# Performance work log

Hardware: AMD Instinct MI355X
Metric: run time of the kernel (lower is better)

The kernel has to match this reference:

```python
import jax, jax.numpy as jnp
import numpy as np

KD = 128; N_STU_TAB = 20000; N_EXER_TAB = 20000
NS = 4096; NE = 4096; NK = 128
E_SE = 131072; E_EK = 16384; B = 8192
ALPHAS = 0.1; ALPHAE = 0.1; TAU = 0.5


def setup_inputs():
    key = jax.random.key(0)
    ks = jax.random.split(key, 32)
    f = lambda i, shape, s=0.09: jax.random.normal(ks[i], shape, dtype=jnp.float32) * s
    ri = lambda i, shape, hi: jax.random.randint(ks[i], shape, 0, hi)
    inp = {
        'E_stu': f(0, (N_STU_TAB, KD), 0.1),
        'E_exer': f(1, (N_EXER_TAB, KD), 0.1),
        'E_k': f(2, (NK, KD), 0.1),
        'W1': f(3, (KD, KD)), 'a1s': f(4, (KD,)), 'a1d': f(5, (KD,)),
        'W2': f(6, (KD, KD)), 'a2s': f(7, (KD,)), 'a2d': f(8, (KD,)),
        'pW1': f(9, (KD, KD)), 'pW2': f(10, (KD, KD)),
        'pW3': f(11, (KD, KD)), 'pb3': jnp.zeros((KD,), jnp.float32),
        'kn_r': (jax.random.uniform(ks[12], (B, KD)) < 0.25).astype(jnp.float32) + 1e-3,
        'stu_ids': ri(13, (NS,), N_STU_TAB),
        'exer_ids': ri(14, (NE,), N_EXER_TAB),
        'k_ids': jnp.arange(NK),
    }
    j = 15
    for g in ('g0', 'g1', 'g2'):
        inp['se_src_' + g] = ri(j, (E_SE,), NS); j += 1
        inp['se_dst_' + g] = ri(j, (E_SE,), NE); j += 1
        inp['ek_src_' + g] = ri(j, (E_EK,), NE); j += 1
        inp['ek_dst_' + g] = ri(j, (E_EK,), NK); j += 1
    inp['stu_index'] = ri(j, (B,), NS); j += 1
    inp['exer_index'] = ri(j, (B,), NE)
    return inp


def _seg_softmax_agg(scores, msgs, dst, n):
    # numerically-stable softmax over edges grouped by destination node
    m = jax.ops.segment_max(scores, dst, num_segments=n)
    m = jnp.where(jnp.isfinite(m), m, 0.0)
    ex = jnp.exp(scores - m[dst])
    den = jax.ops.segment_sum(ex, dst, num_segments=n)
    alpha = ex / (den[dst] + 1e-16)
    return jax.ops.segment_sum(alpha[:, None] * msgs, dst, num_segments=n)


def _gat(emb, edges, W, a_s, a_d):
    # single-head GAT over hetero edges: stu<->exer, exer<->k
    hs, he, hk = emb['stu'] @ W, emb['exer'] @ W, emb['k'] @ W
    ss_s, ss_e, ss_k = hs @ a_s, he @ a_s, hk @ a_s   # src attention terms
    sd_s, sd_e, sd_k = hs @ a_d, he @ a_d, hk @ a_d   # dst attention terms
    se_src, se_dst, ek_src, ek_dst = edges
    lrelu = lambda x: jax.nn.leaky_relu(x, 0.2)
    # stu <- exer (reverse of stu->exer edges)
    sc = lrelu(ss_e[se_dst] + sd_s[se_src])
    new_s = jax.nn.elu(_seg_softmax_agg(sc, he[se_dst], se_src, NS))
    # exer <- stu  and  exer <- k (softmax spans both relations)
    sc1 = lrelu(ss_s[se_src] + sd_e[se_dst])
    sc2 = lrelu(ss_k[ek_dst] + sd_e[ek_src])
    sc = jnp.concatenate([sc1, sc2])
    msg = jnp.concatenate([hs[se_src], hk[ek_dst]])
    dst = jnp.concatenate([se_dst, ek_src])
    new_e = jax.nn.elu(_seg_softmax_agg(sc, msg, dst, NE))
    # k <- exer
    sc = lrelu(ss_e[ek_src] + sd_k[ek_dst])
    new_k = jax.nn.elu(_seg_softmax_agg(sc, he[ek_src], ek_dst, NK))
    return {'stu': new_s, 'exer': new_e, 'k': new_k}


def _closs(h1, h2):
    z1 = h1 / (jnp.linalg.norm(h1, axis=1, keepdims=True) + 1e-12)
    z2 = h2 / (jnp.linalg.norm(h2, axis=1, keepdims=True) + 1e-12)
    sim = z1 @ z2.T                      # [N, N] cosine similarity
    ex = jnp.exp(sim / TAU)
    pos = jnp.diagonal(ex)
    neg = ex.sum(axis=1) - pos           # off-diagonal sum
    return jnp.mean(-jnp.log(pos / (pos + neg)))


def reference(E_stu, E_exer, E_k, W1, a1s, a1d, W2, a2s, a2d,
              pW1, pW2, pW3, pb3, kn_r,
              stu_ids, exer_ids, k_ids,
              se_src_g0, se_dst_g0, ek_src_g0, ek_dst_g0,
              se_src_g1, se_dst_g1, ek_src_g1, ek_dst_g1,
              se_src_g2, se_dst_g2, ek_src_g2, ek_dst_g2,
              stu_index, exer_index):
    e0 = {'stu': E_stu[stu_ids], 'exer': E_exer[exer_ids], 'k': E_k[k_ids]}

    def run(edges):
        e1 = _gat(e0, edges, W1, a1s, a1d)
        return _gat(e1, edges, W2, a2s, a2d)

    main = run((se_src_g0, se_dst_g0, ek_src_g0, ek_dst_g0))
    v1 = run((se_src_g1, se_dst_g1, ek_src_g1, ek_dst_g1))
    v2 = run((se_src_g2, se_dst_g2, ek_src_g2, ek_dst_g2))

    closs = (ALPHAS * (_closs(v1['stu'], v2['stu']) + _closs(v2['stu'], v1['stu']))
             + ALPHAE * (_closs(v1['exer'], v2['exer']) + _closs(v2['exer'], v1['exer'])))

    bs = main['stu'][stu_index]          # [B, KD]
    be = main['exer'][exer_index]        # [B, KD]
    pref = jax.nn.sigmoid(bs @ pW1.T)
    diff = jax.nn.sigmoid(be @ pW2.T)
    o = jax.nn.sigmoid((pref - diff) @ pW3.T + pb3)
    out = (o * kn_r).sum(axis=1) / kn_r.sum(axis=1)
    return out[:, None], closs
```

## Files before the change

### kernel.cpp

```cpp
#include <hip/hip_runtime.h>
#include <hip/hip_bf16.h>
#include <math.h>

#define KD 128
#define NS 4096
#define NE 4096
#define NK 128
#define NNODE (NS + NE + NK)
#define ESE 131072
#define EEK 16384
#define NCSR (2*ESE + 2*EEK)
#define BQ 8192
#define RP (NNODE + 1)
#define HB 32

typedef __attribute__((ext_vector_type(8))) short short8;
typedef __attribute__((ext_vector_type(4))) float float4_;

__device__ __forceinline__ float lrelu_(float x){ return x >= 0.f ? x : 0.2f*x; }
__device__ __forceinline__ float elu_(float x){ return x > 0.f ? x : __expf(x) - 1.f; }
__device__ __forceinline__ float sigm_(float x){ return 1.f/(1.f + __expf(-x)); }
__device__ __forceinline__ float bf2f_(unsigned short u){
  union { unsigned int i; float f; } v; v.i = ((unsigned int)u) << 16; return v.f;
}
__device__ __forceinline__ unsigned short f2b_(float x){
  __hip_bfloat16 b = __float2bfloat16(x); return *(unsigned short*)&b;
}

struct EdgePtrs { const int* s_src[3]; const int* s_dst[3]; const int* e_src[3]; const int* e_dst[3]; };

__global__ __launch_bounds__(256)
void k_fuse1(EdgePtrs ep, int* __restrict__ part,
             const float* __restrict__ W1, const float* __restrict__ a1s,
             const float* __restrict__ a1d,
             unsigned short* __restrict__ hb0, float* __restrict__ ss0,
             float* __restrict__ sd0,
             const float* __restrict__ E_stu, const float* __restrict__ E_exer,
             const float* __restrict__ E_k, const int* __restrict__ sid,
             const int* __restrict__ eid, const int* __restrict__ kid,
             const float* __restrict__ pW1, const float* __restrict__ pW2,
             const float* __restrict__ pW3, float* __restrict__ pWT,
             const float* __restrict__ W2, unsigned short* __restrict__ w2b) {
  __shared__ __align__(16) char smem[NNODE*4];
  int bid = blockIdx.x, t = threadIdx.x;

  if (bid < 3*HB) {
    int* hcnt = (int*)smem;
    int g = bid / HB, b = bid % HB;
    for (int i = t; i < NNODE; i += 256) hcnt[i] = 0;
    __syncthreads();
    const int* ss_ = ep.s_src[g]; const int* sd_ = ep.s_dst[g];
    const int* es_ = ep.e_src[g]; const int* ed_ = ep.e_dst[g];
    int se0 = b*(ESE/HB);
    for (int i = se0 + t; i < se0 + ESE/HB; i += 256) {
      atomicAdd(&hcnt[ss_[i]], 1);
      atomicAdd(&hcnt[NS + sd_[i]], 1);
    }
    int ek0 = b*(EEK/HB);
    for (int i = ek0 + t; i < ek0 + EEK/HB; i += 256) {
      atomicAdd(&hcnt[NS + es_[i]], 1);
      atomicAdd(&hcnt[NS + NE + ed_[i]], 1);
    }
    __syncthreads();
    int* pp = part + ((size_t)g*HB + b)*NNODE;
    for (int i = t; i < NNODE; i += 256) pp[i] = hcnt[i];
    return;
  }

  if (bid < 3*HB + NNODE/32) {
    float (*ers)[KD] = (float(*)[KD])smem;
    int row0 = (bid - 3*HB)*32;
    int w = t >> 6, c = t & 63;
    for (int i = t; i < 32*KD; i += 256) {
      int r = i >> 7, k = i & 127;
      int gr = row0 + r;
      const float* srow;
      if (gr < NS)           srow = E_stu  + (size_t)sid[gr]*KD;
      else if (gr < NS + NE) srow = E_exer + (size_t)eid[gr - NS]*KD;
      else                   srow = E_k    + (size_t)kid[gr - NS - NE]*KD;
      ers[r][k] = srow[k];
    }
    __syncthreads();
    float acc0[8] = {0,0,0,0,0,0,0,0}, acc1[8] = {0,0,0,0,0,0,0,0};
    #pragma unroll 2
    for (int kc = 0; kc < KD; kc += 4) {
      float wa[4], wb[4];
      #pragma unroll
      for (int j = 0; j < 4; j++) {
        wa[j] = W1[(kc + j)*KD + c];
        wb[j] = W1[(kc + j)*KD + c + 64];
      }
      #pragma unroll
      for (int r = 0; r < 8; r++) {
        float4 e = *(const float4*)&ers[w*8 + r][kc];
        acc0[r] += e.x*wa[0] + e.y*wa[1] + e.z*wa[2] + e.w*wa[3];
        acc1[r] += e.x*wb[0] + e.y*wb[1] + e.z*wb[2] + e.w*wb[3];
      }
    }
    float as1 = a1s[c], as2 = a1s[c + 64], ad1 = a1d[c], ad2 = a1d[c + 64];
    #pragma unroll
    for (int r = 0; r < 8; r++) {
      int gr = row0 + w*8 + r;
      hb0[(size_t)gr*KD + c]      = f2b_(acc0[r]);
      hb0[(size_t)gr*KD + c + 64] = f2b_(acc1[r]);
      float s = acc0[r]*as1 + acc1[r]*as2;
      float d = acc0[r]*ad1 + acc1[r]*ad2;
      #pragma unroll
      for (int off = 32; off; off >>= 1) { s += __shfl_xor(s, off); d += __shfl_xor(d, off); }
      if (c == 0) { ss0[gr] = s; sd0[gr] = d; }
    }
    return;
  }

  {
    float (*tile)[33] = (float(*)[33])smem;
    int idx = bid - 3*HB - NNODE/32;
    int tx = t & 31, ty = t >> 5;
    if (idx < 48) {
      int m = idx >> 4, rem = idx & 15;
      int bx = (rem & 3)*32, by = (rem >> 2)*32;
      const float* src = m == 0 ? pW1 : (m == 1 ? pW2 : pW3);
      float* dst = pWT + m*KD*KD;
      for (int j = 0; j < 32; j += 8)
        tile[ty + j][tx] = src[(by + ty + j)*KD + bx + tx];
      __syncthreads();
      for (int j = 0; j < 32; j += 8)
        dst[(bx + ty + j)*KD + by + tx] = tile[tx][ty + j];
    } else {
      int rem = idx - 48;
      int bx = (rem & 3)*32, by = (rem >> 2)*32;
      for (int j = 0; j < 32; j += 8)
        tile[ty + j][tx] = W2[(by + ty + j)*KD + bx + tx];
      __syncthreads();
      for (int j = 0; j < 32; j += 8)
        w2b[(bx + ty + j)*KD + by + tx] = f2b_(tile[tx][ty + j]);
    }
  }
}

__global__ void k_sumpart(const int* __restrict__ part, int* __restrict__ cnt_all) {
  int idx = blockIdx.x*256 + threadIdx.x;
  if (idx >= 3*NNODE) return;
  int g = idx / NNODE, n = idx - g*NNODE;
  const int* pg = part + (size_t)g*HB*NNODE + n;
  int s = 0;
  #pragma unroll
  for (int b = 0; b < HB; b++) s += pg[(size_t)b*NNODE];
  cnt_all[idx] = s;
}

__global__ void k_scan(const int* __restrict__ cnt_all, int* __restrict__ rp_all) {
  __shared__ int sums[1024];
  const int CH = (NNODE + 1023) / 1024;
  int g = blockIdx.x, t = threadIdx.x;
  const int* cnt = cnt_all + g*NNODE;
  int* row_ptr = rp_all + g*RP;
  int base = t*CH;
  int local[CH];
  int s = 0;
  for (int j = 0; j < CH; j++) {
    int v = (base + j < NNODE) ? cnt[base + j] : 0;
    local[j] = s; s += v;
  }
  sums[t] = s; __syncthreads();
  for (int off = 1; off < 1024; off <<= 1) {
    int v = (t >= off) ? sums[t - off] : 0;
    __syncthreads();
    sums[t] += v;
    __syncthreads();
  }
  int excl = (t == 0) ? 0 : sums[t - 1];
  for (int j = 0; j < CH; j++)
    if (base + j < NNODE) row_ptr[base + j] = excl + local[j];
  if (t == 1023) row_ptr[NNODE] = sums[1023];
}

__global__ void k_boff(const int* __restrict__ part, const int* __restrict__ rp_all,
                       int* __restrict__ boff) {
  int idx = blockIdx.x*256 + threadIdx.x;
  if (idx >= 3*NNODE) return;
  int g = idx / NNODE, n = idx - g*NNODE;
  const int* pg = part + (size_t)g*HB*NNODE + n;
  int* bg = boff + (size_t)g*HB*NNODE + n;
  int acc = rp_all[g*RP + n];
  #pragma unroll
  for (int b = 0; b < HB; b++) {
    bg[(size_t)b*NNODE] = acc;
    acc += pg[(size_t)b*NNODE];
  }
}

__global__ __launch_bounds__(256)
void k_scatter(EdgePtrs ep, const int* __restrict__ boff, unsigned short* __restrict__ col_all) {
  __shared__ int cur[NNODE];
  int g = blockIdx.y, b = blockIdx.x, t = threadIdx.x;
  const int* bg = boff + ((size_t)g*HB + b)*NNODE;
  for (int i = t; i < NNODE; i += 256) cur[i] = bg[i];
  __syncthreads();
  const int* ss_ = ep.s_src[g]; const int* sd_ = ep.s_dst[g];
  const int* es_ = ep.e_src[g]; const int* ed_ = ep.e_dst[g];
  unsigned short* col = col_all + (size_t)g*NCSR;
  int se0 = b*(ESE/HB);
  for (int i = se0 + t; i < se0 + ESE/HB; i += 256) {
    int s = ss_[i], d = NS + sd_[i];
    col[atomicAdd(&cur[s], 1)] = (unsigned short)d;
    col[atomicAdd(&cur[d], 1)] = (unsigned short)s;
  }
  int ek0 = b*(EEK/HB);
  for (int i = ek0 + t; i < ek0 + EEK/HB; i += 256) {
    int s = NS + es_[i], d = NS + NE + ed_[i];
    col[atomicAdd(&cur[s], 1)] = (unsigned short)d;
    col[atomicAdd(&cur[d], 1)] = (unsigned short)s;
  }
}

__global__ __launch_bounds__(256)
void k_mgemm(const unsigned short* __restrict__ X, const unsigned short* __restrict__ WT,
             const float* __restrict__ a_s, const float* __restrict__ a_d,
             unsigned short* __restrict__ hb, float* __restrict__ ss,
             float* __restrict__ sd) {
  __shared__ unsigned short As[128*KD];
  __shared__ unsigned short Bs[128*KD];
  __shared__ float ssp[128][2], sdp[128][2];
  int t = threadIdx.x;
  const unsigned short* Arow = X + (size_t)blockIdx.x*128*KD;
  #pragma unroll
  for (int j = 0; j < 8; j++) {
    int G = t + j*256;
    int r = G >> 4, g = G & 15;
    int sw = g ^ (r & 15);
    *(float4*)&As[(r*16 + sw)*8] = *(const float4*)&Arow[(size_t)G*8];
    *(float4*)&Bs[(r*16 + sw)*8] = *(const float4*)&WT[(size_t)G*8];
  }
  __syncthreads();
  int w = t >> 6, lane = t & 63;
  int rw = (w >> 1)*64, cw = (w & 1)*64;
  int m15 = lane & 15, quad = lane >> 4;
  float4_ acc[4][4] = {};
  #pragma unroll
  for (int kq = 0; kq < 4; kq++) {
    short8 a[4], b[4];
    int g = kq*4 + quad;
    #pragma unroll
    for (int mi = 0; mi < 4; mi++) {
      int r = rw + mi*16 + m15;
      a[mi] = *(const short8*)&As[(r*16 + (g ^ (r & 15)))*8];
    }
    #pragma unroll
    for (int ni = 0; ni < 4; ni++) {
      int r = cw + ni*16 + m15;
      b[ni] = *(const short8*)&Bs[(r*16 + (g ^ (r & 15)))*8];
    }
    #pragma unroll
    for (int mi = 0; mi < 4; mi++)
      #pragma unroll
      for (int ni = 0; ni < 4; ni++)
        acc[mi][ni] = __builtin_amdgcn_mfma_f32_16x16x32_bf16(a[mi], b[ni], acc[mi][ni], 0, 0, 0);
  }
  int row0 = blockIdx.x*128;
  float asv[4], adv[4];
  #pragma unroll
  for (int ni = 0; ni < 4; ni++) {
    int gc = cw + ni*16 + m15;
    asv[ni] = a_s[gc]; adv[ni] = a_d[gc];
  }
  #pragma unroll
  for (int mi = 0; mi < 4; mi++) {
    #pragma unroll
    for (int reg = 0; reg < 4; reg++) {
      int lr = rw + mi*16 + quad*4 + reg;
      int gr = row0 + lr;
      float s = 0.f, d = 0.f;
      #pragma unroll
      for (int ni = 0; ni < 4; ni++) {
        float v = acc[mi][ni][reg];
        hb[(size_t)gr*KD + cw + ni*16 + m15] = f2b_(v);
        s += v*asv[ni]; d += v*adv[ni];
      }
      s += __shfl_xor(s, 1); d += __shfl_xor(d, 1);
      s += __shfl_xor(s, 2); d += __shfl_xor(d, 2);
      s += __shfl_xor(s, 4); d += __shfl_xor(d, 4);
      s += __shfl_xor(s, 8); d += __shfl_xor(d, 8);
      if (m15 == 0) { ssp[lr][w & 1] = s; sdp[lr][w & 1] = d; }
    }
  }
  __syncthreads();
  if (t < 128) {
    ss[row0 + t] = ssp[t][0] + ssp[t][1];
    sd[row0 + t] = sdp[t][0] + sdp[t][1];
  }
}

__global__ __launch_bounds__(256)
void k_head(const float* __restrict__ Wa, const float* __restrict__ Wb,
            const float* __restrict__ Wc,
            const float* __restrict__ pb, const float* __restrict__ knr,
            float* __restrict__ out, const float* __restrict__ pbuf,
            const float* __restrict__ g1,
            const int* __restrict__ i1, const int* __restrict__ i2) {
  constexpr int ROWS = 32, RPW = 8;
  __shared__ float ers[ROWS][KD];
  __shared__ float xs[ROWS][KD];
  int t = threadIdx.x;
  int row0 = blockIdx.x * ROWS;
  int w = t >> 6, c = t & 63;

  for (int i = t; i < ROWS*KD; i += 256) {
    int r = i >> 7, k = i & 127;
    ers[r][k] = g1[(size_t)i1[row0 + r]*KD + k];
  }
  __syncthreads();

  float acc0[RPW], acc1[RPW];
  #pragma unroll
  for (int r = 0; r < RPW; r++) { acc0[r] = 0.f; acc1[r] = 0.f; }
  #pragma unroll 2
  for (int kc = 0; kc < KD; kc += 4) {
    float wa[4], wb[4];
    #pragma unroll
    for (int j = 0; j < 4; j++) {
      wa[j] = Wa[(kc + j)*KD + c];
      wb[j] = Wa[(kc + j)*KD + c + 64];
    }
    #pragma unroll
    for (int r = 0; r < RPW; r++) {
      float4 e = *(const float4*)&ers[w*RPW + r][kc];
      acc0[r] += e.x*wa[0] + e.y*wa[1] + e.z*wa[2] + e.w*wa[3];
      acc1[r] += e.x*wb[0] + e.y*wb[1] + e.z*wb[2] + e.w*wb[3];
    }
  }
  #pragma unroll
  for (int r = 0; r < RPW; r++) {
    xs[w*RPW + r][c]      = sigm_(acc0[r]);
    xs[w*RPW + r][c + 64] = sigm_(acc1[r]);
  }
  __syncthreads();
  for (int i = t; i < ROWS*KD; i += 256) {
    int r = i >> 7, k = i & 127;
    ers[r][k] = g1[(size_t)(NS + i2[row0 + r])*KD + k];
  }
  __syncthreads();
  #pragma unroll
  for (int r = 0; r < RPW; r++) { acc0[r] = 0.f; acc1[r] = 0.f; }
  #pragma unroll 2
  for (int kc = 0; kc < KD; kc += 4) {
    float wa[4], wb[4];
    #pragma unroll
    for (int j = 0; j < 4; j++) {
      wa[j] = Wb[(kc + j)*KD + c];
      wb[j] = Wb[(kc + j)*KD + c + 64];
    }
    #pragma unroll
    for (int r = 0; r < RPW; r++) {
      float4 e = *(const float4*)&ers[w*RPW + r][kc];
      acc0[r] += e.x*wa[0] + e.y*wa[1] + e.z*wa[2] + e.w*wa[3];
      acc1[r] += e.x*wb[0] + e.y*wb[1] + e.z*wb[2] + e.w*wb[3];
    }
  }
  #pragma unroll
  for (int r = 0; r < RPW; r++) {
    xs[w*RPW + r][c]      -= sigm_(acc0[r]);
    xs[w*RPW + r][c + 64] -= sigm_(acc1[r]);
  }
  #pragma unroll
  for (int r = 0; r < RPW; r++) { acc0[r] = 0.f; acc1[r] = 0.f; }
  #pragma unroll 2
  for (int kc = 0; kc < KD; kc += 4) {
    float wa[4], wb[4];
    #pragma unroll
    for (int j = 0; j < 4; j++) {
      wa[j] = Wc[(kc + j)*KD + c];
      wb[j] = Wc[(kc + j)*KD + c + 64];
    }
    #pragma unroll
    for (int r = 0; r < RPW; r++) {
      float4 e = *(const float4*)&xs[w*RPW + r][kc];
      acc0[r] += e.x*wa[0] + e.y*wa[1] + e.z*wa[2] + e.w*wa[3];
      acc1[r] += e.x*wb[0] + e.y*wb[1] + e.z*wb[2] + e.w*wb[3];
    }
  }
  float b1 = pb[c], b2 = pb[c + 64];
  #pragma unroll
  for (int r = 0; r < RPW; r++) {
    int gr = row0 + w*RPW + r;
    float kr1 = knr[(size_t)gr*KD + c], kr2 = knr[(size_t)gr*KD + c + 64];
    float o1 = sigm_(acc0[r] + b1), o2 = sigm_(acc1[r] + b2);
    float num = o1*kr1 + o2*kr2, den = kr1 + kr2;
    #pragma unroll
    for (int off = 32; off; off >>= 1) { num += __shfl_xor(num, off); den += __shfl_xor(den, off); }
    if (c == 0) out[gr] = num/den;
  }
  if (blockIdx.x == 0 && w == 0) {
    int lane = t & 63;
    float v = (lane < 32) ? pbuf[lane] : 0.f;
    #pragma unroll
    for (int off = 32; off; off >>= 1) v += __shfl_xor(v, off);
    if (lane == 0) out[BQ] = 0.1f*v/(float)NS;
  }
}

__global__ __launch_bounds__(256)
void k_agg(const int* __restrict__ rp_all, const unsigned short* __restrict__ col_all,
           const unsigned short* __restrict__ hb_base, const float* __restrict__ ss,
           const float* __restrict__ sd, unsigned short* __restrict__ outb,
           float* __restrict__ out, unsigned short* __restrict__ Zo, int gsel) {
  int wv = blockIdx.x*4 + (threadIdx.x >> 6);
  int lane = threadIdx.x & 63;
  if (wv >= 3*NNODE) return;
  int g = wv / NNODE, node = wv - g*NNODE;
  bool layer2 = (gsel == -2);
  if (layer2 && node >= NS + NE) return;
  const int* rp = rp_all + g*RP;
  const unsigned short* cl = col_all + (size_t)g*NCSR;
  const unsigned short* hgb = layer2 ? hb_base + (size_t)g*NNODE*KD : hb_base;
  const float* ssg = layer2 ? ss + g*NNODE : ss;
  const float* sdg = layer2 ? sd + g*NNODE : sd;
  int e0 = rp[node], e1 = rp[node + 1];
  float sdv = sdg[node];
  int sub = lane >> 4;
  int fl  = lane & 15;
  float l = 0.f;
  float A[8] = {0,0,0,0,0,0,0,0};
  #pragma unroll 4
  for (int e = e0 + sub; e < e1; e += 4) {
    int o = cl[e];
    float pj = __expf(lrelu_(ssg[o] + sdv));
    l += pj;
    short8 mv = *(const short8*)&hgb[(size_t)o*KD + fl*8];
    #pragma unroll
    for (int q = 0; q < 8; q++)
      A[q] += pj * bf2f_((unsigned short)mv[q]);
  }
  l += __shfl_xor(l, 16); l += __shfl_xor(l, 32);
  #pragma unroll
  for (int q = 0; q < 8; q++) {
    A[q] += __shfl_xor(A[q], 16);
    A[q] += __shfl_xor(A[q], 32);
  }
  float inv = 1.f/(l + 1e-16f);
  float av[8];
  #pragma unroll
  for (int q = 0; q < 8; q++) av[q] = elu_(A[q]*inv);
  if (!layer2) {
    if (sub == 0) {
      short8 sv;
      #pragma unroll
      for (int q = 0; q < 8; q++) sv[q] = (short)f2b_(av[q]);
      *(short8*)&outb[(size_t)wv*KD + fl*8] = sv;
    }
    return;
  }
  if (g == 0) {
    if (sub == 0) {
      float* orow = &out[(size_t)node*KD + fl*8];
      *(float4*)orow       = make_float4(av[0], av[1], av[2], av[3]);
      *(float4*)(orow + 4) = make_float4(av[4], av[5], av[6], av[7]);
    }
  } else {
    float nrm = av[0]*av[0] + av[1]*av[1] + av[2]*av[2] + av[3]*av[3]
              + av[4]*av[4] + av[5]*av[5] + av[6]*av[6] + av[7]*av[7];
    #pragma unroll
    for (int off = 1; off <= 8; off <<= 1) nrm += __shfl_xor(nrm, off);
    float invn = 1.f/(sqrtf(nrm) + 1e-12f);
    if (sub == 0) {
      short8 sv;
      #pragma unroll
      for (int q = 0; q < 8; q++) sv[q] = (short)f2b_(av[q]*invn);
      *(short8*)&Zo[((size_t)(g - 1)*8192 + node)*KD + fl*8] = sv;
    }
  }
}

__global__ __launch_bounds__(256)
void k_sim(const unsigned short* __restrict__ Z, float* __restrict__ rsp,
           float* __restrict__ csp, float* __restrict__ dg_all) {
  __shared__ unsigned short As[128*KD];
  __shared__ unsigned short Bs[128*KD];
  int z = blockIdx.z;
  int t = threadIdx.x;
  const unsigned short* Arow = Z + ((size_t)z*NS + (size_t)blockIdx.x*128)*KD;
  const unsigned short* Brow = Z + ((size_t)8192 + (size_t)z*NS + (size_t)blockIdx.y*128)*KD;
  #pragma unroll
  for (int j = 0; j < 8; j++) {
    int G = t + j*256;
    int r = G >> 4, g = G & 15;
    int sw = g ^ (r & 15);
    *(float4*)&As[(r*16 + sw)*8] = *(const float4*)&Arow[(size_t)G*8];
    *(float4*)&Bs[(r*16 + sw)*8] = *(const float4*)&Brow[(size_t)G*8];
  }
  __syncthreads();
  int w = t >> 6, lane = t & 63;
  int rw = (w >> 1)*64, cw = (w & 1)*64;
  int m15 = lane & 15, quad = lane >> 4;
  float4_ acc[4][4] = {};
  #pragma unroll
  for (int kq = 0; kq < 4; kq++) {
    short8 a[4], b[4];
    int g = kq*4 + quad;
    #pragma unroll
    for (int mi = 0; mi < 4; mi++) {
      int r = rw + mi*16 + m15;
      a[mi] = *(const short8*)&As[(r*16 + (g ^ (r & 15)))*8];
    }
    #pragma unroll
    for (int ni = 0; ni < 4; ni++) {
      int r = cw + ni*16 + m15;
      b[ni] = *(const short8*)&Bs[(r*16 + (g ^ (r & 15)))*8];
    }
    #pragma unroll
    for (int mi = 0; mi < 4; mi++)
      #pragma unroll
      for (int ni = 0; ni < 4; ni++)
        acc[mi][ni] = __builtin_amdgcn_mfma_f32_16x16x32_bf16(a[mi], b[ni], acc[mi][ni], 0, 0, 0);
  }
  int i0 = blockIdx.x*128, j0 = blockIdx.y*128;
  float* diag = dg_all + z*NS;
  float* rrow = rsp + ((size_t)z*64 + blockIdx.y*2 + (w & 1))*NS;
  float* crow = csp + ((size_t)z*64 + blockIdx.x*2 + (w >> 1))*NS;
  float cs[4] = {0,0,0,0};
  #pragma unroll
  for (int mi = 0; mi < 4; mi++) {
    float rs[4] = {0,0,0,0};
    #pragma unroll
    for (int ni = 0; ni < 4; ni++) {
      #pragma unroll
      for (int reg = 0; reg < 4; reg++) {
        float sim2 = acc[mi][ni][reg]*2.0f;
        int gi = i0 + rw + mi*16 + quad*4 + reg;
        int gj = j0 + cw + ni*16 + m15;
        if (gi == gj) diag[gi] = sim2;
        float e = __expf(sim2);
        rs[reg] += e; cs[ni] += e;
      }
    }
    #pragma unroll
    for (int reg = 0; reg < 4; reg++) {
      float v = rs[reg];
      v += __shfl_xor(v, 1); v += __shfl_xor(v, 2);
      v += __shfl_xor(v, 4); v += __shfl_xor(v, 8);
      if (m15 == 0) rrow[i0 + rw + mi*16 + quad*4 + reg] = v;
    }
  }
  #pragma unroll
  for (int ni = 0; ni < 4; ni++) {
    float v = cs[ni];
    v += __shfl_xor(v, 16); v += __shfl_xor(v, 32);
    if (quad == 0) crow[j0 + cw + ni*16 + m15] = v;
  }
}

__global__ void k_lred(const float* __restrict__ rsp, const float* __restrict__ csp,
                       const float* __restrict__ dg_all, float* __restrict__ pbuf) {
  __shared__ float red[256];
  int z = blockIdx.y;
  int i = blockIdx.x*256 + threadIdx.x;
  float rs = 0.f, cs = 0.f;
  for (int s = 0; s < 64; s++) {
    rs += rsp[((size_t)z*64 + s)*NS + i];
    cs += csp[((size_t)z*64 + s)*NS + i];
  }
  float v = logf(rs) + logf(cs) - 2.f*dg_all[z*NS + i];
  red[threadIdx.x] = v; __syncthreads();
  for (int off = 128; off; off >>= 1) {
    if (threadIdx.x < off) red[threadIdx.x] += red[threadIdx.x + off];
    __syncthreads();
  }
  if (threadIdx.x == 0) pbuf[z*16 + blockIdx.x] = red[0];
}

extern "C" void kernel_launch(void* const* d_in, const int* in_sizes, int n_in,
                              void* d_out, int out_size, void* d_ws, size_t ws_size,
                              hipStream_t stream) {
  const float* E_stu  = (const float*)d_in[0];
  const float* E_exer = (const float*)d_in[1];
  const float* E_k    = (const float*)d_in[2];
  const float* W1  = (const float*)d_in[3];
  const float* a1s = (const float*)d_in[4];
  const float* a1d = (const float*)d_in[5];
  const float* W2  = (const float*)d_in[6];
  const float* a2s = (const float*)d_in[7];
  const float* a2d = (const float*)d_in[8];
  const float* pW1 = (const float*)d_in[9];
  const float* pW2 = (const float*)d_in[10];
  const float* pW3 = (const float*)d_in[11];
  const float* pb3 = (const float*)d_in[12];
  const float* kn_r = (const float*)d_in[13];
  const int* stu_ids  = (const int*)d_in[14];
  const int* exer_ids = (const int*)d_in[15];
  const int* k_ids    = (const int*)d_in[16];
  EdgePtrs ep;
  for (int g = 0; g < 3; g++) {
    ep.s_src[g] = (const int*)d_in[17 + g*4];
    ep.s_dst[g] = (const int*)d_in[18 + g*4];
    ep.e_src[g] = (const int*)d_in[19 + g*4];
    ep.e_dst[g] = (const int*)d_in[20 + g*4];
  }
  const int* stu_index  = (const int*)d_in[29];
  const int* exer_index = (const int*)d_in[30];
  float* out = (float*)d_out;

  char* p = (char*)d_ws;
  auto carve = [&](size_t bytes) -> char* {
    char* r = p; p += (bytes + 255) & ~(size_t)255; return r;
  };
  const size_t NODE_F = (size_t)NNODE*KD;
  float* ssb = (float*)carve((size_t)8*NNODE*4);
  float* ss0 = ssb,            *sd0 = ssb + NNODE;
  float* ss3 = ssb + 2*NNODE,  *sd3 = ssb + 5*NNODE;
  unsigned short* hb0 = (unsigned short*)carve(NODE_F*2);
  unsigned short* hb3 = (unsigned short*)carve(3*NODE_F*2);
  char* Creg = carve((size_t)8*HB*NNODE*4);
  int*   part = (int*)Creg;
  int*   boff = (int*)Creg + (size_t)3*HB*NNODE;
  unsigned short* etb = (unsigned short*)Creg;
  float* eoutAll = (float*)carve((size_t)(NS + NE)*KD*4);
  int* cnt_all = (int*)carve((size_t)3*NNODE*4);
  int* rp_all  = (int*)carve((size_t)3*RP*4);
  unsigned short* col_all = (unsigned short*)carve((size_t)3*NCSR*2);
  float* pWT = (float*)carve((size_t)3*KD*KD*4);
  float* pW1T = pWT, *pW2T = pWT + KD*KD, *pW3T = pWT + 2*KD*KD;
  float* rsp = (float*)carve((size_t)2*64*NS*4);
  float* csp = (float*)carve((size_t)2*64*NS*4);
  float* dg_all = (float*)carve((size_t)2*NS*4);
  float* pbuf = (float*)carve(64*4);
  unsigned short* Z = (unsigned short*)carve((size_t)2*8192*KD*2);
  unsigned short* w2b = (unsigned short*)carve((size_t)KD*KD*2);

  k_fuse1<<<3*HB + NNODE/32 + 48 + 16, 256, 0, stream>>>(
      ep, part, W1, a1s, a1d, hb0, ss0, sd0,
      E_stu, E_exer, E_k, stu_ids, exer_ids, k_ids,
      pW1, pW2, pW3, pWT, W2, w2b);

  k_sumpart<<<(3*NNODE + 255)/256, 256, 0, stream>>>(part, cnt_all);
  k_scan<<<3, 1024, 0, stream>>>(cnt_all, rp_all);
  k_boff<<<(3*NNODE + 255)/256, 256, 0, stream>>>(part, rp_all, boff);
  k_scatter<<<dim3(HB, 3), 256, 0, stream>>>(ep, boff, col_all);

  k_agg<<<3*NNODE/4, 256, 0, stream>>>(rp_all, col_all, hb0, ss0, sd0, etb,
                                       nullptr, nullptr, -1);

  k_mgemm<<<3*NNODE/128, 256, 0, stream>>>(etb, w2b, a2s, a2d, hb3, ss3, sd3);
  k_agg<<<3*NNODE/4, 256, 0, stream>>>(rp_all, col_all, hb3, ss3, sd3, nullptr,
                                       eoutAll, Z, -2);

  k_sim<<<dim3(32, 32, 2), 256, 0, stream>>>(Z, rsp, csp, dg_all);
  k_lred<<<dim3(16, 2), 256, 0, stream>>>(rsp, csp, dg_all, pbuf);

  k_head<<<BQ/32, 256, 0, stream>>>(pW1T, pW2T, pW3T, pb3, kn_r,
                                    out, pbuf, eoutAll, stu_index, exer_index);
}
```

Baseline: 307.7 us.

## Rewrite prediction head as bf16 MFMA GEMMs with swizzled LDS tiles

Replaces the scalar fp32 FMA prediction head with a kernel that runs the three 128x128 projections on bf16 MFMA 16x16x32 instructions. The gathered student and exercise rows are converted to bf16 into XOR-swizzled shared-memory tiles. The head weights are now converted to bf16 in their original row-major layout instead of being transposed in fp32. This cuts ALU work in the head, but the head is a small slice of total time and bf16 rounding adds some error.

```diff
diff --git a/kernel.cpp b/kernel.cpp
--- a/kernel.cpp
+++ b/kernel.cpp
@@ -15,6 +15,7 @@
 #define HB 32
 
 typedef __attribute__((ext_vector_type(8))) short short8;
+typedef __attribute__((ext_vector_type(4))) short short4_;
 typedef __attribute__((ext_vector_type(4))) float float4_;
 
 __device__ __forceinline__ float lrelu_(float x){ return x >= 0.f ? x : 0.2f*x; }
@@ -39,7 +40,7 @@
              const float* __restrict__ E_k, const int* __restrict__ sid,
              const int* __restrict__ eid, const int* __restrict__ kid,
              const float* __restrict__ pW1, const float* __restrict__ pW2,
-             const float* __restrict__ pW3, float* __restrict__ pWT,
+             const float* __restrict__ pW3, unsigned short* __restrict__ pWb,
              const float* __restrict__ W2, unsigned short* __restrict__ w2b) {
   __shared__ __align__(16) char smem[NNODE*4];
   int bid = blockIdx.x, t = threadIdx.x;
@@ -113,27 +114,28 @@
   }
 
   {
-    float (*tile)[33] = (float(*)[33])smem;
     int idx = bid - 3*HB - NNODE/32;
-    int tx = t & 31, ty = t >> 5;
-    if (idx < 48) {
-      int m = idx >> 4, rem = idx & 15;
-      int bx = (rem & 3)*32, by = (rem >> 2)*32;
-      const float* src = m == 0 ? pW1 : (m == 1 ? pW2 : pW3);
-      float* dst = pWT + m*KD*KD;
-      for (int j = 0; j < 32; j += 8)
-        tile[ty + j][tx] = src[(by + ty + j)*KD + bx + tx];
-      __syncthreads();
-      for (int j = 0; j < 32; j += 8)
-        dst[(bx + ty + j)*KD + by + tx] = tile[tx][ty + j];
-    } else {
-      int rem = idx - 48;
-      int bx = (rem & 3)*32, by = (rem >> 2)*32;
+    if (idx < 16) {
+      float (*tile)[33] = (float(*)[33])smem;
+      int tx = t & 31, ty = t >> 5;
+      int bx = (idx & 3)*32, by = (idx >> 2)*32;
       for (int j = 0; j < 32; j += 8)
         tile[ty + j][tx] = W2[(by + ty + j)*KD + bx + tx];
       __syncthreads();
       for (int j = 0; j < 32; j += 8)
         w2b[(bx + ty + j)*KD + by + tx] = f2b_(tile[tx][ty + j]);
+    } else {
+      int r = idx - 16;
+      const float* src = r < 4 ? pW1 : (r < 8 ? pW2 : pW3);
+      unsigned short* dst = pWb + (size_t)(r >> 2)*KD*KD;
+      int off = (r & 3)*4096;
+      for (int i = t; i < 1024; i += 256) {
+        float4 v = *(const float4*)&src[off + i*4];
+        short4_ s;
+        s[0] = (short)f2b_(v.x); s[1] = (short)f2b_(v.y);
+        s[2] = (short)f2b_(v.z); s[3] = (short)f2b_(v.w);
+        *(short4_*)&dst[off + i*4] = s;
+      }
     }
   }
 }
@@ -292,106 +294,113 @@
 }
 
 __global__ __launch_bounds__(256)
-void k_head(const float* __restrict__ Wa, const float* __restrict__ Wb,
-            const float* __restrict__ Wc,
-            const float* __restrict__ pb, const float* __restrict__ knr,
-            float* __restrict__ out, const float* __restrict__ pbuf,
-            const float* __restrict__ g1,
-            const int* __restrict__ i1, const int* __restrict__ i2) {
-  constexpr int ROWS = 32, RPW = 8;
-  __shared__ float ers[ROWS][KD];
-  __shared__ float xs[ROWS][KD];
+void k_headm(const unsigned short* __restrict__ pWb,
+             const float* __restrict__ pb, const float* __restrict__ knr,
+             float* __restrict__ out, const float* __restrict__ pbuf,
+             const float* __restrict__ g1,
+             const int* __restrict__ i1, const int* __restrict__ i2) {
+  __shared__ unsigned short At[32*KD];
+  __shared__ unsigned short Bt[32*KD];
+  __shared__ unsigned short Xt[32*KD];
+  __shared__ float nump[32][2], denp[32][2];
   int t = threadIdx.x;
-  int row0 = blockIdx.x * ROWS;
-  int w = t >> 6, c = t & 63;
-
-  for (int i = t; i < ROWS*KD; i += 256) {
-    int r = i >> 7, k = i & 127;
-    ers[r][k] = g1[(size_t)i1[row0 + r]*KD + k];
+  int row0 = blockIdx.x*32;
+  for (int i = t; i < 512; i += 256) {
+    int r = i >> 4, g = i & 15;
+    int sw = g ^ (r & 15);
+    {
+      const float* src = &g1[(size_t)i1[row0 + r]*KD + g*8];
+      float4 v0 = *(const float4*)src, v1 = *(const float4*)(src + 4);
+      short8 s;
+      s[0] = (short)f2b_(v0.x); s[1] = (short)f2b_(v0.y);
+      s[2] = (short)f2b_(v0.z); s[3] = (short)f2b_(v0.w);
+      s[4] = (short)f2b_(v1.x); s[5] = (short)f2b_(v1.y);
+      s[6] = (short)f2b_(v1.z); s[7] = (short)f2b_(v1.w);
+      *(short8*)&At[(r*16 + sw)*8] = s;
+    }
+    {
+      const float* src = &g1[(size_t)(NS + i2[row0 + r])*KD + g*8];
+      float4 v0 = *(const float4*)src, v1 = *(const float4*)(src + 4);
+      short8 s;
+      s[0] = (short)f2b_(v0.x); s[1] = (short)f2b_(v0.y);
+      s[2] = (short)f2b_(v0.z); s[3] = (short)f2b_(v0.w);
+      s[4] = (short)f2b_(v1.x); s[5] = (short)f2b_(v1.y);
+      s[6] = (short)f2b_(v1.z); s[7] = (short)f2b_(v1.w);
+      *(short8*)&Bt[(r*16 + sw)*8] = s;
+    }
   }
   __syncthreads();
-
-  float acc0[RPW], acc1[RPW];
-  #pragma unroll
-  for (int r = 0; r < RPW; r++) { acc0[r] = 0.f; acc1[r] = 0.f; }
-  #pragma unroll 2
-  for (int kc = 0; kc < KD; kc += 4) {
-    float wa[4], wb[4];
-    #pragma unroll
-    for (int j = 0; j < 4; j++) {
-      wa[j] = Wa[(kc + j)*KD + c];
-      wb[j] = Wa[(kc + j)*KD + c + 64];
-    }
-    #pragma unroll
-    for (int r = 0; r < RPW; r++) {
-      float4 e = *(const float4*)&ers[w*RPW + r][kc];
-      acc0[r] += e.x*wa[0] + e.y*wa[1] + e.z*wa[2] + e.w*wa[3];
-      acc1[r] += e.x*wb[0] + e.y*wb[1] + e.z*wb[2] + e.w*wb[3];
-    }
-  }
-  #pragma unroll
-  for (int r = 0; r < RPW; r++) {
-    xs[w*RPW + r][c]      = sigm_(acc0[r]);
-    xs[w*RPW + r][c + 64] = sigm_(acc1[r]);
+  int w = t >> 6, lane = t & 63;
+  int rw = (w >> 1)*16, cw = (w & 1)*64;
+  int m15 = lane & 15, quad = lane >> 4;
+  const unsigned short* W1g = pWb;
+  const unsigned short* W2g = pWb + KD*KD;
+  const unsigned short* W3g = pWb + 2*KD*KD;
+  float4_ accP[4] = {}, accD[4] = {};
+  #pragma unroll
+  for (int kq = 0; kq < 4; kq++) {
+    int g = kq*4 + quad;
+    int ra = rw + m15;
+    short8 a1 = *(const short8*)&At[(ra*16 + (g ^ (ra & 15)))*8];
+    short8 a2 = *(const short8*)&Bt[(ra*16 + (g ^ (ra & 15)))*8];
+    #pragma unroll
+    for (int ni = 0; ni < 4; ni++) {
+      int rb = cw + ni*16 + m15;
+      short8 b1 = *(const short8*)&W1g[(size_t)rb*KD + g*8];
+      short8 b2 = *(const short8*)&W2g[(size_t)rb*KD + g*8];
+      accP[ni] = __builtin_amdgcn_mfma_f32_16x16x32_bf16(a1, b1, accP[ni], 0, 0, 0);
+      accD[ni] = __builtin_amdgcn_mfma_f32_16x16x32_bf16(a2, b2, accD[ni], 0, 0, 0);
+    }
+  }
+  #pragma unroll
+  for (int ni = 0; ni < 4; ni++) {
+    #pragma unroll
+    for (int reg = 0; reg < 4; reg++) {
+      int lr = rw + quad*4 + reg;
+      int col = cw + ni*16 + m15;
+      float diff = sigm_(accP[ni][reg]) - sigm_(accD[ni][reg]);
+      int g2 = col >> 3;
+      Xt[(lr*16 + (g2 ^ (lr & 15)))*8 + (col & 7)] = f2b_(diff);
+    }
   }
   __syncthreads();
-  for (int i = t; i < ROWS*KD; i += 256) {
-    int r = i >> 7, k = i & 127;
-    ers[r][k] = g1[(size_t)(NS + i2[row0 + r])*KD + k];
+  float4_ accO[4] = {};
+  #pragma unroll
+  for (int kq = 0; kq < 4; kq++) {
+    int g = kq*4 + quad;
+    int ra = rw + m15;
+    short8 a = *(const short8*)&Xt[(ra*16 + (g ^ (ra & 15)))*8];
+    #pragma unroll
+    for (int ni = 0; ni < 4; ni++) {
+      int rb = cw + ni*16 + m15;
+      short8 b = *(const short8*)&W3g[(size_t)rb*KD + g*8];
+      accO[ni] = __builtin_amdgcn_mfma_f32_16x16x32_bf16(a, b, accO[ni], 0, 0, 0);
+    }
+  }
+  float pbv[4];
+  #pragma unroll
+  for (int ni = 0; ni < 4; ni++) pbv[ni] = pb[cw + ni*16 + m15];
+  #pragma unroll
+  for (int reg = 0; reg < 4; reg++) {
+    int lr = rw + quad*4 + reg;
+    int gr = row0 + lr;
+    float num = 0.f, den = 0.f;
+    #pragma unroll
+    for (int ni = 0; ni < 4; ni++) {
+      float kr = knr[(size_t)gr*KD + cw + ni*16 + m15];
+      float o = sigm_(accO[ni][reg] + pbv[ni]);
+      num += o*kr; den += kr;
+    }
+    num += __shfl_xor(num, 1); den += __shfl_xor(den, 1);
+    num += __shfl_xor(num, 2); den += __shfl_xor(den, 2);
+    num += __shfl_xor(num, 4); den += __shfl_xor(den, 4);
+    num += __shfl_xor(num, 8); den += __shfl_xor(den, 8);
+    if (m15 == 0) { nump[lr][w & 1] = num; denp[lr][w & 1] = den; }
   }
   __syncthreads();
-  #pragma unroll
-  for (int r = 0; r < RPW; r++) { acc0[r] = 0.f; acc1[r] = 0.f; }
-  #pragma unroll 2
-  for (int kc = 0; kc < KD; kc += 4) {
-    float wa[4], wb[4];
-    #pragma unroll
-    for (int j = 0; j < 4; j++) {
-      wa[j] = Wb[(kc + j)*KD + c];
-      wb[j] = Wb[(kc + j)*KD + c + 64];
-    }
-    #pragma unroll
-    for (int r = 0; r < RPW; r++) {
-      float4 e = *(const float4*)&ers[w*RPW + r][kc];
-      acc0[r] += e.x*wa[0] + e.y*wa[1] + e.z*wa[2] + e.w*wa[3];
-      acc1[r] += e.x*wb[0] + e.y*wb[1] + e.z*wb[2] + e.w*wb[3];
-    }
-  }
-  #pragma unroll
-  for (int r = 0; r < RPW; r++) {
-    xs[w*RPW + r][c]      -= sigm_(acc0[r]);
-    xs[w*RPW + r][c + 64] -= sigm_(acc1[r]);
-  }
-  #pragma unroll
-  for (int r = 0; r < RPW; r++) { acc0[r] = 0.f; acc1[r] = 0.f; }
-  #pragma unroll 2
-  for (int kc = 0; kc < KD; kc += 4) {
-    float wa[4], wb[4];
-    #pragma unroll
-    for (int j = 0; j < 4; j++) {
-      wa[j] = Wc[(kc + j)*KD + c];
-      wb[j] = Wc[(kc + j)*KD + c + 64];
-    }
-    #pragma unroll
-    for (int r = 0; r < RPW; r++) {
-      float4 e = *(const float4*)&xs[w*RPW + r][kc];
-      acc0[r] += e.x*wa[0] + e.y*wa[1] + e.z*wa[2] + e.w*wa[3];
-      acc1[r] += e.x*wb[0] + e.y*wb[1] + e.z*wb[2] + e.w*wb[3];
-    }
-  }
-  float b1 = pb[c], b2 = pb[c + 64];
-  #pragma unroll
-  for (int r = 0; r < RPW; r++) {
-    int gr = row0 + w*RPW + r;
-    float kr1 = knr[(size_t)gr*KD + c], kr2 = knr[(size_t)gr*KD + c + 64];
-    float o1 = sigm_(acc0[r] + b1), o2 = sigm_(acc1[r] + b2);
-    float num = o1*kr1 + o2*kr2, den = kr1 + kr2;
-    #pragma unroll
-    for (int off = 32; off; off >>= 1) { num += __shfl_xor(num, off); den += __shfl_xor(den, off); }
-    if (c == 0) out[gr] = num/den;
-  }
+  if (t < 32)
+    out[row0 + t] = (nump[t][0] + nump[t][1]) / (denp[t][0] + denp[t][1]);
   if (blockIdx.x == 0 && w == 0) {
-    int lane = t & 63;
     float v = (lane < 32) ? pbuf[lane] : 0.f;
     #pragma unroll
     for (int off = 32; off; off >>= 1) v += __shfl_xor(v, off);
@@ -617,8 +626,7 @@
   int* cnt_all = (int*)carve((size_t)3*NNODE*4);
   int* rp_all  = (int*)carve((size_t)3*RP*4);
   unsigned short* col_all = (unsigned short*)carve((size_t)3*NCSR*2);
-  float* pWT = (float*)carve((size_t)3*KD*KD*4);
-  float* pW1T = pWT, *pW2T = pWT + KD*KD, *pW3T = pWT + 2*KD*KD;
+  unsigned short* pWb = (unsigned short*)carve((size_t)3*KD*KD*2);
   float* rsp = (float*)carve((size_t)2*64*NS*4);
   float* csp = (float*)carve((size_t)2*64*NS*4);
   float* dg_all = (float*)carve((size_t)2*NS*4);
@@ -626,10 +634,10 @@
   unsigned short* Z = (unsigned short*)carve((size_t)2*8192*KD*2);
   unsigned short* w2b = (unsigned short*)carve((size_t)KD*KD*2);
 
-  k_fuse1<<<3*HB + NNODE/32 + 48 + 16, 256, 0, stream>>>(
+  k_fuse1<<<3*HB + NNODE/32 + 16 + 12, 256, 0, stream>>>(
       ep, part, W1, a1s, a1d, hb0, ss0, sd0,
       E_stu, E_exer, E_k, stu_ids, exer_ids, k_ids,
-      pW1, pW2, pW3, pWT, W2, w2b);
+      pW1, pW2, pW3, pWb, W2, w2b);
 
   k_sumpart<<<(3*NNODE + 255)/256, 256, 0, stream>>>(part, cnt_all);
   k_scan<<<3, 1024, 0, stream>>>(cnt_all, rp_all);
@@ -646,6 +654,6 @@
   k_sim<<<dim3(32, 32, 2), 256, 0, stream>>>(Z, rsp, csp, dg_all);
   k_lred<<<dim3(16, 2), 256, 0, stream>>>(rsp, csp, dg_all, pbuf);
 
-  k_head<<<BQ/32, 256, 0, stream>>>(pW1T, pW2T, pW3T, pb3, kn_r,
-                                    out, pbuf, eoutAll, stu_index, exer_index);
-}
+  k_headm<<<BQ/32, 256, 0, stream>>>(pWb, pb3, kn_r,
+                                     out, pbuf, eoutAll, stu_index, exer_index);
+}
```

After: 275.2 us. 10.6% less time.
